# Kernel tuning notes

Hardware: AMD Instinct MI355X
Metric: run time of the kernel (lower is better)

## Reference

```python
import math
import jax, jax.numpy as jnp
import numpy as np

B, N, M = 8, 2048, 1024
INPUT_SIZE = 512
HEAD_DIM = 64
NUM_HEADS = 6
ATTN_SIZE = HEAD_DIM * NUM_HEADS
MAX_CLASSES = 512


def setup_inputs() -> dict:
    key = jax.random.key(0)
    k1, k2, k3, k4, k5, k6, k7 = jax.random.split(key, 7)
    bound = 1.0 / math.sqrt(INPUT_SIZE)
    return {
        "train_embeddings": jax.random.normal(k1, (B, N, INPUT_SIZE), jnp.float32),
        "test_embeddings": jax.random.normal(k2, (B, M, INPUT_SIZE), jnp.float32),
        "targets": jax.random.randint(k3, (B, N), 0, MAX_CLASSES),
        # torch nn.Linear weights, stored as [in, out] for direct matmul
        "Wq": jax.random.uniform(k4, (INPUT_SIZE, ATTN_SIZE), jnp.float32, -bound, bound),
        "bq": jax.random.uniform(k5, (ATTN_SIZE,), jnp.float32, -bound, bound),
        "Wk": jax.random.uniform(k6, (INPUT_SIZE, ATTN_SIZE), jnp.float32, -bound, bound),
        "bk": jax.random.uniform(k7, (ATTN_SIZE,), jnp.float32, -bound, bound),
    }


def reference(train_embeddings, test_embeddings, targets, Wq, bq, Wk, bk):
    b, m, _ = test_embeddings.shape
    # projections -> [B, S, H, D]
    q_bmhd = (test_embeddings @ Wq + bq).reshape(b, m, NUM_HEADS, HEAD_DIM)
    k_bnhd = (train_embeddings @ Wk + bk).reshape(b, -1, NUM_HEADS, HEAD_DIM)
    scale = 1.0 / math.sqrt(HEAD_DIM)  # SDPA default scale
    # attention scores [B, H, M, N]
    scores = jnp.einsum("bmhd,bnhd->bhmn", q_bmhd, k_bnhd) * scale
    attn = jax.nn.softmax(scores, axis=-1)
    # one-hot train targets [B, N, C]; chunk-folding in the torch code is a
    # memory trick — mathematically it is just attn @ one_hot per head
    onehot_bnc = jax.nn.one_hot(targets, MAX_CLASSES, dtype=q_bmhd.dtype)
    out_bhmc = jnp.einsum("bhmn,bnc->bhmc", attn, onehot_bnc)
    out_bmc = out_bhmc.mean(axis=1)          # mean over heads
    out_mbc = out_bmc.transpose(1, 0, 2)      # [M, B, C]
    return jnp.log(jnp.clip(out_mbc, 1e-05) + 3e-05)
```

## Files before the change

### kernel.cpp

```cpp
#include <hip/hip_runtime.h>
#include <hip/hip_bf16.h>

#define BQ 8
#define NN 2048
#define MM 1024
#define EE 512
#define NH 6
#define AA 384
#define CC 512

#define KROW_B (AA * 2)
#define TILE_B (16 * KROW_B)
#define STILE_B (32 * KROW_B)
#define WROW_B (EE * 2)
#define WTILE_B (16 * WROW_B)

#define QSCALE 0.1803368801111204f

typedef __bf16 bf16x8 __attribute__((ext_vector_type(8)));
typedef float  f32x4  __attribute__((ext_vector_type(4)));
using bf16 = __hip_bfloat16;

static __device__ __forceinline__ f32x4 mfma16(bf16x8 a, bf16x8 b, f32x4 c) {
  return __builtin_amdgcn_mfma_f32_16x16x32_bf16(a, b, c, 0, 0, 0);
}

typedef __attribute__((address_space(1))) const void gconst_void;
typedef __attribute__((address_space(3))) void lds_void_t;
static __device__ __forceinline__ void ld_lds16(const void* g, void* l) {
  __builtin_amdgcn_global_load_lds((gconst_void*)g, (lds_void_t*)l, 16, 0, 0);
}

static __device__ __forceinline__ unsigned short f2bfu(float x) {
  union { __hip_bfloat16 h; unsigned short u; } v;
  v.h = __float2bfloat16(x);
  return v.u;
}
static __device__ __forceinline__ float bf2f(unsigned short u) {
  union { unsigned int i; float f; } x;
  x.i = ((unsigned int)u) << 16;
  return x.f;
}

__global__ __launch_bounds__(512) void prep_kernel(
    const float* __restrict__ Wq, const float* __restrict__ Wk,
    bf16* __restrict__ WqT, bf16* __restrict__ WkT,
    const int* __restrict__ targets, int* __restrict__ cnts, int* __restrict__ idxP)
{
  __shared__ float t[64][65];
  __shared__ int cnt[CC], pos[CC];
  int bid = blockIdx.x, tid = threadIdx.x;
  if (bid < 96) {
    if (tid >= 256) { __syncthreads(); return; }
    int id = bid;
    const float* W = (id < 48) ? Wq : Wk;
    bf16* WT = (id < 48) ? WqT : WkT;
    if (id >= 48) id -= 48;
    int kb = (id / 6) * 64, nb = (id % 6) * 64;
    int lr = tid >> 4, lc = (tid & 15) * 4;
    #pragma unroll
    for (int p = 0; p < 4; p++) {
      int k = lr + p * 16;
      float4 v = *reinterpret_cast<const float4*>(W + (size_t)(kb + k) * AA + nb + lc);
      t[k][lc] = v.x; t[k][lc + 1] = v.y; t[k][lc + 2] = v.z; t[k][lc + 3] = v.w;
    }
    __syncthreads();
    #pragma unroll
    for (int p = 0; p < 4; p++) {
      int n = lr + p * 16;
      bf16* dst = WT + (size_t)(nb + n) * EE + kb + lc;
      dst[0] = __float2bfloat16(t[lc][n]);
      dst[1] = __float2bfloat16(t[lc + 1][n]);
      dst[2] = __float2bfloat16(t[lc + 2][n]);
      dst[3] = __float2bfloat16(t[lc + 3][n]);
    }
    return;
  }
  int b = bid - 96;
  cnt[tid] = 0;
  pos[tid] = 0;
  int4 sent = make_int4(NN, NN, NN, NN);
  int4* prow = reinterpret_cast<int4*>(idxP + ((size_t)b * CC + tid) * 32);
  #pragma unroll
  for (int i = 0; i < 8; i++) prow[i] = sent;
  __syncthreads();
  int tv[4];
  #pragma unroll
  for (int i = 0; i < 4; i++) {
    tv[i] = targets[b * NN + tid * 4 + i];
    atomicAdd(&cnt[tv[i]], 1);
  }
  __syncthreads();
  cnts[b * CC + tid] = cnt[tid];
  __syncthreads();
  #pragma unroll
  for (int i = 0; i < 4; i++) {
    int p = atomicAdd(&pos[tv[i]], 1);
    if (p < 32) idxP[((size_t)b * CC + tv[i]) * 32 + p] = tid * 4 + i;
  }
}

__global__ __launch_bounds__(256, 3) void proj_kernel(
    const float* __restrict__ test, const float* __restrict__ train,
    const bf16* __restrict__ WqT, const bf16* __restrict__ WkT,
    const float* __restrict__ bq, const float* __restrict__ bk,
    bf16* __restrict__ Qb, bf16* __restrict__ Kb)
{
  __shared__ char wbuf[3][WTILE_B];
  int tid = threadIdx.x, wid = tid >> 6, lane = tid & 63;
  int bid = blockIdx.x;
  int sub = bid & 1, unit = bid >> 1;
  const float* A; const bf16* WT; const float* bias; bf16* C; float scale; int m0;
  if (unit < 128) { A = test;  WT = WqT; bias = bq; C = Qb; scale = QSCALE; m0 = unit * 64; }
  else            { A = train; WT = WkT; bias = bk; C = Kb; scale = 1.0f;   m0 = (unit - 128) * 64; }
  m0 += wid * 16;
  int row = lane & 15, hi = lane >> 4;

  bf16x8 af[16];
  const float* arow = A + (size_t)(m0 + row) * EE + hi * 8;
  #pragma unroll
  for (int ks = 0; ks < 16; ks++) {
    float4 u = *reinterpret_cast<const float4*>(arow + ks * 32);
    float4 v = *reinterpret_cast<const float4*>(arow + ks * 32 + 4);
    bf16x8 f;
    f[0] = (__bf16)u.x; f[1] = (__bf16)u.y; f[2] = (__bf16)u.z; f[3] = (__bf16)u.w;
    f[4] = (__bf16)v.x; f[5] = (__bf16)v.y; f[6] = (__bf16)v.z; f[7] = (__bf16)v.w;
    af[ks] = f;
  }

  int ldso[4], srco[4];
  #pragma unroll
  for (int i = 0; i < 4; i++) {
    int off = tid * 16 + i * 4096;
    int rw = off >> 10, c = off & 1023;
    ldso[i] = off;
    srco[i] = rw * WROW_B + (c ^ ((rw & 7) << 4));
  }
  const char* wgbase = (const char*)WT + (size_t)sub * 12 * WTILE_B;
  int sw = (row & 7) << 4;

  auto stage = [&](int t, int buf) {
    const char* src = wgbase + (size_t)t * WTILE_B;
    #pragma unroll
    for (int i = 0; i < 4; i++) ld_lds16(src + srco[i], wbuf[buf] + ldso[i]);
  };
  auto compute = [&](int buf, int t) {
    const char* wb = wbuf[buf] + row * WROW_B;
    f32x4 acc0 = {0.f, 0.f, 0.f, 0.f}, acc1 = {0.f, 0.f, 0.f, 0.f};
    #pragma unroll
    for (int ks = 0; ks < 16; ks += 2) {
      bf16x8 w0 = *reinterpret_cast<const bf16x8*>(wb + ((hi * 16 + ks * 64) ^ sw));
      bf16x8 w1 = *reinterpret_cast<const bf16x8*>(wb + ((hi * 16 + (ks + 1) * 64) ^ sw));
      acc0 = mfma16(af[ks], w0, acc0);
      acc1 = mfma16(af[ks + 1], w1, acc1);
    }
    f32x4 acc = acc0 + acc1;
    int ocol = (sub * 12 + t) * 16 + row;
    float bv = bias[ocol];
    #pragma unroll
    for (int j = 0; j < 4; j++)
      C[(size_t)(m0 + hi * 4 + j) * AA + ocol] = __float2bfloat16((acc[j] + bv) * scale);
  };

  stage(0, 0);
  stage(1, 1);
  asm volatile("s_waitcnt vmcnt(4)" ::: "memory");
  __builtin_amdgcn_s_barrier();
  __builtin_amdgcn_sched_barrier(0);
  stage(2, 2);
  compute(0, 0);

  int cur = 1, stg = 0;
  #pragma unroll 1
  for (int t = 1; t < 11; t++) {
    asm volatile("s_waitcnt vmcnt(8)" ::: "memory");
    __builtin_amdgcn_s_barrier();
    __builtin_amdgcn_sched_barrier(0);
    if (t < 10) stage(t + 2, stg);
    compute(cur, t);
    cur = cur + 1 < 3 ? cur + 1 : 0;
    stg = stg + 1 < 3 ? stg + 1 : 0;
  }
  asm volatile("s_waitcnt vmcnt(4)" ::: "memory");
  __builtin_amdgcn_s_barrier();
  __builtin_amdgcn_sched_barrier(0);
  compute(cur, 11);
}

__global__ __launch_bounds__(256, 2) void zpass_kernel(
    const bf16* __restrict__ Qb, const bf16* __restrict__ Kb, float* __restrict__ Zp)
{
  __shared__ char kbuf[2][STILE_B];
  int id = blockIdx.x;
  int b = id & 7, r = id >> 3, mt = r & 7, nc = r >> 3;
  int tid = threadIdx.x, wid = tid >> 6, lane = tid & 63;
  int m0 = mt * 128 + wid * 32, n0 = nc * 256;
  int row = lane & 15, hi = lane >> 4;

  bf16x8 qf[2][12];
  #pragma unroll
  for (int s = 0; s < 2; s++) {
    const bf16* qrow = Qb + ((size_t)(b * MM + m0 + s * 16 + row)) * AA + hi * 8;
    #pragma unroll
    for (int ks = 0; ks < 12; ks++) qf[s][ks] = *reinterpret_cast<const bf16x8*>(qrow + ks * 32);
  }

  int ldso[6], srco[6];
  #pragma unroll
  for (int i = 0; i < 6; i++) {
    int off = tid * 16 + i * 4096;
    int rw = off / KROW_B, c = off - rw * KROW_B;
    ldso[i] = off;
    srco[i] = rw * KROW_B + (c ^ ((rw & 7) << 4));
  }
  const char* kgbase = (const char*)(Kb + ((size_t)(b * NN + n0)) * AA);

  int sw = (row & 7) << 4;
  int rbase = row * KROW_B;
  int x0 = rbase + ((hi * 16) ^ sw);
  int x1 = rbase + (((hi * 16) + 64) ^ sw);

  float zacc[2][NH][4];
  #pragma unroll
  for (int s = 0; s < 2; s++)
    #pragma unroll
    for (int h = 0; h < NH; h++)
      #pragma unroll
      for (int j = 0; j < 4; j++) zacc[s][h][j] = 0.f;

  auto stage = [&](int t, int buf) {
    const char* src = kgbase + (size_t)t * STILE_B;
    #pragma unroll
    for (int i = 0; i < 6; i++) ld_lds16(src + srco[i], kbuf[buf] + ldso[i]);
  };
  auto compute = [&](int buf) {
    __builtin_amdgcn_s_setprio(1);
    #pragma unroll
    for (int sub = 0; sub < 2; sub++) {
      const char* kb = kbuf[buf] + sub * TILE_B;
      #pragma unroll
      for (int h = 0; h < NH; h++) {
        bf16x8 k0 = *reinterpret_cast<const bf16x8*>(kb + h * 128 + x0);
        bf16x8 k1 = *reinterpret_cast<const bf16x8*>(kb + h * 128 + x1);
        f32x4 a0 = {0.f, 0.f, 0.f, 0.f}, a1 = {0.f, 0.f, 0.f, 0.f};
        a0 = mfma16(qf[0][2 * h], k0, a0);
        a1 = mfma16(qf[1][2 * h], k0, a1);
        a0 = mfma16(qf[0][2 * h + 1], k1, a0);
        a1 = mfma16(qf[1][2 * h + 1], k1, a1);
        #pragma unroll
        for (int j = 0; j < 4; j++) {
          zacc[0][h][j] += __builtin_amdgcn_exp2f(a0[j]);
          zacc[1][h][j] += __builtin_amdgcn_exp2f(a1[j]);
        }
      }
    }
    __builtin_amdgcn_s_setprio(0);
  };

  stage(0, 0);
  asm volatile("s_waitcnt vmcnt(0)" ::: "memory");
  __builtin_amdgcn_s_barrier();
  __builtin_amdgcn_sched_barrier(0);
  stage(1, 1);
  compute(0);

  #pragma unroll 1
  for (int i = 1; i < 8; i++) {
    asm volatile("s_waitcnt vmcnt(0)" ::: "memory");
    __builtin_amdgcn_s_barrier();
    __builtin_amdgcn_sched_barrier(0);
    if (i < 7) stage(i + 1, (i + 1) & 1);
    compute(i & 1);
  }

  #pragma unroll
  for (int s = 0; s < 2; s++)
    #pragma unroll
    for (int h = 0; h < NH; h++)
      #pragma unroll
      for (int j = 0; j < 4; j++) {
        float v = zacc[s][h][j];
        v += __shfl_xor(v, 1); v += __shfl_xor(v, 2);
        v += __shfl_xor(v, 4); v += __shfl_xor(v, 8);
        zacc[s][h][j] = v;
      }
  if (row == 0) {
    #pragma unroll
    for (int s = 0; s < 2; s++)
      #pragma unroll
      for (int h = 0; h < NH; h++)
        #pragma unroll
        for (int j = 0; j < 4; j++)
          Zp[(((size_t)nc * 8 + b) * NH + h) * MM + m0 + s * 16 + hi * 4 + j] = zacc[s][h][j];
  }
}

__global__ __launch_bounds__(256, 2) void wpass_kernel(
    const bf16* __restrict__ Qb, const bf16* __restrict__ Kb,
    const float* __restrict__ Zp, bf16* __restrict__ W2)
{
  __shared__ char kbuf[2][STILE_B];
  int id = blockIdx.x;
  int b = id & 7, r = id >> 3, mt = r & 7, nc = r >> 3;
  int tid = threadIdx.x, wid = tid >> 6, lane = tid & 63;
  int m0 = mt * 128 + wid * 32, n0 = nc * 256;
  int row = lane & 15, hi = lane >> 4;

  bf16x8 qf[2][12];
  #pragma unroll
  for (int s = 0; s < 2; s++) {
    const bf16* qrow = Qb + ((size_t)(b * MM + m0 + s * 16 + row)) * AA + hi * 8;
    #pragma unroll
    for (int ks = 0; ks < 12; ks++) qf[s][ks] = *reinterpret_cast<const bf16x8*>(qrow + ks * 32);
  }

  f32x4 lrz4[2][NH];
  #pragma unroll
  for (int s = 0; s < 2; s++)
    #pragma unroll
    for (int h = 0; h < NH; h++) {
      f32x4 z = {0.f, 0.f, 0.f, 0.f};
      #pragma unroll
      for (int p = 0; p < 8; p++)
        z += *reinterpret_cast<const f32x4*>(Zp + (((size_t)p * 8 + b) * NH + h) * MM + m0 + s * 16 + hi * 4);
      f32x4 l;
      #pragma unroll
      for (int j = 0; j < 4; j++) l[j] = -__log2f(6.0f * z[j]);
      lrz4[s][h] = l;
    }

  int ldso[6], srco[6];
  #pragma unroll
  for (int i = 0; i < 6; i++) {
    int off = tid * 16 + i * 4096;
    int rw = off / KROW_B, c = off - rw * KROW_B;
    ldso[i] = off;
    srco[i] = rw * KROW_B + (c ^ ((rw & 7) << 4));
  }
  const char* kgbase = (const char*)(Kb + ((size_t)(b * NN + n0)) * AA);

  int sw = (row & 7) << 4;
  int rbase = row * KROW_B;
  int x0 = rbase + ((hi * 16) ^ sw);
  int x1 = rbase + (((hi * 16) + 64) ^ sw);

  int m4a = (m0 >> 2) + hi;
  int m4b = ((m0 + 16) >> 2) + hi;

  auto stage = [&](int t, int buf) {
    const char* src = kgbase + (size_t)t * STILE_B;
    #pragma unroll
    for (int i = 0; i < 6; i++) ld_lds16(src + srco[i], kbuf[buf] + ldso[i]);
  };
  auto compute = [&](int buf, int st) {
    #pragma unroll
    for (int sub = 0; sub < 2; sub++) {
      const char* kb = kbuf[buf] + sub * TILE_B;
      __builtin_amdgcn_s_setprio(1);
      float w0a = 0.f, w1a = 0.f, w2a = 0.f, w3a = 0.f;
      float w0b = 0.f, w1b = 0.f, w2b = 0.f, w3b = 0.f;
      #pragma unroll
      for (int h = 0; h < NH; h++) {
        bf16x8 k0 = *reinterpret_cast<const bf16x8*>(kb + h * 128 + x0);
        bf16x8 k1 = *reinterpret_cast<const bf16x8*>(kb + h * 128 + x1);
        f32x4 a0 = mfma16(qf[0][2 * h], k0, lrz4[0][h]);
        f32x4 a1 = mfma16(qf[1][2 * h], k0, lrz4[1][h]);
        a0 = mfma16(qf[0][2 * h + 1], k1, a0);
        a1 = mfma16(qf[1][2 * h + 1], k1, a1);
        w0a += __builtin_amdgcn_exp2f(a0[0]);
        w1a += __builtin_amdgcn_exp2f(a0[1]);
        w2a += __builtin_amdgcn_exp2f(a0[2]);
        w3a += __builtin_amdgcn_exp2f(a0[3]);
        w0b += __builtin_amdgcn_exp2f(a1[0]);
        w1b += __builtin_amdgcn_exp2f(a1[1]);
        w2b += __builtin_amdgcn_exp2f(a1[2]);
        w3b += __builtin_amdgcn_exp2f(a1[3]);
      }
      __builtin_amdgcn_s_setprio(0);
      int n = n0 + (st * 2 + sub) * 16 + row;
      ushort4 qa, qb2;
      qa.x = f2bfu(w0a); qa.y = f2bfu(w1a); qa.z = f2bfu(w2a); qa.w = f2bfu(w3a);
      qb2.x = f2bfu(w0b); qb2.y = f2bfu(w1b); qb2.z = f2bfu(w2b); qb2.w = f2bfu(w3b);
      *reinterpret_cast<ushort4*>((unsigned short*)W2 + (((size_t)(b * 256 + m4a)) * NN + n) * 4) = qa;
      *reinterpret_cast<ushort4*>((unsigned short*)W2 + (((size_t)(b * 256 + m4b)) * NN + n) * 4) = qb2;
    }
  };

  stage(0, 0);
  asm volatile("s_waitcnt vmcnt(0)" ::: "memory");
  __builtin_amdgcn_s_barrier();
  __builtin_amdgcn_sched_barrier(0);
  stage(1, 1);
  compute(0, 0);

  #pragma unroll 1
  for (int i = 1; i < 8; i++) {
    asm volatile("s_waitcnt vmcnt(4)" ::: "memory");
    __builtin_amdgcn_s_barrier();
    __builtin_amdgcn_sched_barrier(0);
    if (i < 7) stage(i + 1, (i + 1) & 1);
    compute(i & 1, i);
  }
}

__global__ __launch_bounds__(512) void gather_kernel(
    const bf16* __restrict__ W2, const int* __restrict__ cnts,
    const int* __restrict__ idxP, float* __restrict__ out)
{
  __shared__ char wl[2 * (NN + 1) * 8];
  int id = blockIdx.x;
  int b = id & 7, mt = id >> 3;
  int g0 = mt * 2;
  int tid = threadIdx.x;

  #pragma unroll
  for (int g = 0; g < 2; g++) {
    const uint4* src = (const uint4*)((const unsigned short*)W2 + ((size_t)(b * 256 + g0 + g)) * NN * 4);
    uint4* dst = (uint4*)(wl + g * (NN + 1) * 8);
    #pragma unroll
    for (int i = tid; i < NN * 8 / 16; i += 512) dst[i] = src[i];
  }
  if (tid < 2) *reinterpret_cast<unsigned long long*>(wl + tid * (NN + 1) * 8 + NN * 8) = 0ull;
  __syncthreads();

  int c = tid;
  int cnt = cnts[b * CC + c];
  const int* ip = idxP + ((size_t)b * CC + c) * 32;
  #pragma unroll 1
  for (int g = 0; g < 2; g++) {
    const char* base = wl + g * (NN + 1) * 8;
    float s0 = 0.f, s1 = 0.f, s2 = 0.f, s3 = 0.f;
    #pragma unroll 1
    for (int i = 0; i < cnt; i += 8) {
      int4 ia = *reinterpret_cast<const int4*>(ip + i);
      int4 ib = *reinterpret_cast<const int4*>(ip + i + 4);
      ushort4 v0 = *reinterpret_cast<const ushort4*>(base + ia.x * 8);
      ushort4 v1 = *reinterpret_cast<const ushort4*>(base + ia.y * 8);
      ushort4 v2 = *reinterpret_cast<const ushort4*>(base + ia.z * 8);
      ushort4 v3 = *reinterpret_cast<const ushort4*>(base + ia.w * 8);
      ushort4 v4 = *reinterpret_cast<const ushort4*>(base + ib.x * 8);
      ushort4 v5 = *reinterpret_cast<const ushort4*>(base + ib.y * 8);
      ushort4 v6 = *reinterpret_cast<const ushort4*>(base + ib.z * 8);
      ushort4 v7 = *reinterpret_cast<const ushort4*>(base + ib.w * 8);
      s0 += bf2f(v0.x) + bf2f(v1.x) + bf2f(v2.x) + bf2f(v3.x) + bf2f(v4.x) + bf2f(v5.x) + bf2f(v6.x) + bf2f(v7.x);
      s1 += bf2f(v0.y) + bf2f(v1.y) + bf2f(v2.y) + bf2f(v3.y) + bf2f(v4.y) + bf2f(v5.y) + bf2f(v6.y) + bf2f(v7.y);
      s2 += bf2f(v0.z) + bf2f(v1.z) + bf2f(v2.z) + bf2f(v3.z) + bf2f(v4.z) + bf2f(v5.z) + bf2f(v6.z) + bf2f(v7.z);
      s3 += bf2f(v0.w) + bf2f(v1.w) + bf2f(v2.w) + bf2f(v3.w) + bf2f(v4.w) + bf2f(v5.w) + bf2f(v6.w) + bf2f(v7.w);
    }
    int m = mt * 8 + g * 4;
    out[((size_t)(m + 0) * BQ + b) * CC + c] = __logf(fmaxf(s0, 1e-5f) + 3e-5f);
    out[((size_t)(m + 1) * BQ + b) * CC + c] = __logf(fmaxf(s1, 1e-5f) + 3e-5f);
    out[((size_t)(m + 2) * BQ + b) * CC + c] = __logf(fmaxf(s2, 1e-5f) + 3e-5f);
    out[((size_t)(m + 3) * BQ + b) * CC + c] = __logf(fmaxf(s3, 1e-5f) + 3e-5f);
  }
}

extern "C" void kernel_launch(void* const* d_in, const int* in_sizes, int n_in,
                              void* d_out, int out_size, void* d_ws, size_t ws_size,
                              hipStream_t stream) {
  const float* train = (const float*)d_in[0];
  const float* test  = (const float*)d_in[1];
  const int*   tgt   = (const int*)d_in[2];
  const float* Wq    = (const float*)d_in[3];
  const float* bq    = (const float*)d_in[4];
  const float* Wk    = (const float*)d_in[5];
  const float* bk    = (const float*)d_in[6];
  float* out = (float*)d_out;

  char* ws = (char*)d_ws;
  bf16*  WqT  = (bf16*)(ws);
  bf16*  WkT  = (bf16*)(ws + 393216);
  bf16*  Qb   = (bf16*)(ws + 786432);
  bf16*  Kb   = (bf16*)(ws + 7077888);
  float* Zp   = (float*)(ws + 19660800);
  bf16*  Wbuf = (bf16*)(ws + 21233664);
  int*   cnts = (int*)(ws + 54788096);
  int*   idxP = (int*)(ws + 54804480);

  prep_kernel<<<104, 512, 0, stream>>>(Wq, Wk, WqT, WkT, tgt, cnts, idxP);
  proj_kernel<<<768, 256, 0, stream>>>(test, train, WqT, WkT, bq, bk, Qb, Kb);
  zpass_kernel<<<512, 256, 0, stream>>>(Qb, Kb, Zp);
  wpass_kernel<<<512, 256, 0, stream>>>(Qb, Kb, Zp, Wbuf);
  gather_kernel<<<1024, 512, 0, stream>>>(Wbuf, cnts, idxP, out);
}
```

Measured before the change: 107.3 us.

## Shrink zpass/wpass blocks to 2 waves with triple-buffered 16-row K tiles

The zpass and wpass kernels now launch twice as many blocks of 128 threads, each covering 64 query rows instead of 128. Each iteration stages a 16-row K tile instead of 32 rows, over a 3-deep LDS ring with partial vmcnt waits, so loads run two tiles ahead of compute. The aim is more resident blocks, finer-grained barriers and better latency hiding. The cost is that each K tile is reloaded by twice as many blocks, raising global/L2 traffic for K.

```diff
diff --git a/kernel.cpp b/kernel.cpp
--- a/kernel.cpp
+++ b/kernel.cpp
@@ -11,7 +11,6 @@
 
 #define KROW_B (AA * 2)
 #define TILE_B (16 * KROW_B)
-#define STILE_B (32 * KROW_B)
 #define WROW_B (EE * 2)
 #define WTILE_B (16 * WROW_B)
 
@@ -187,14 +186,14 @@
   compute(cur, 11);
 }
 
-__global__ __launch_bounds__(256, 2) void zpass_kernel(
+__global__ __launch_bounds__(128) void zpass_kernel(
     const bf16* __restrict__ Qb, const bf16* __restrict__ Kb, float* __restrict__ Zp)
 {
-  __shared__ char kbuf[2][STILE_B];
+  __shared__ char kbuf[3][TILE_B];
   int id = blockIdx.x;
-  int b = id & 7, r = id >> 3, mt = r & 7, nc = r >> 3;
+  int b = id & 7, r = id >> 3, mt = r & 15, nc = r >> 4;
   int tid = threadIdx.x, wid = tid >> 6, lane = tid & 63;
-  int m0 = mt * 128 + wid * 32, n0 = nc * 256;
+  int m0 = mt * 64 + wid * 32, n0 = nc * 256;
   int row = lane & 15, hi = lane >> 4;
 
   bf16x8 qf[2][12];
@@ -208,7 +207,7 @@
   int ldso[6], srco[6];
   #pragma unroll
   for (int i = 0; i < 6; i++) {
-    int off = tid * 16 + i * 4096;
+    int off = tid * 16 + i * 2048;
     int rw = off / KROW_B, c = off - rw * KROW_B;
     ldso[i] = off;
     srco[i] = rw * KROW_B + (c ^ ((rw & 7) << 4));
@@ -229,49 +228,54 @@
       for (int j = 0; j < 4; j++) zacc[s][h][j] = 0.f;
 
   auto stage = [&](int t, int buf) {
-    const char* src = kgbase + (size_t)t * STILE_B;
+    const char* src = kgbase + (size_t)t * TILE_B;
     #pragma unroll
     for (int i = 0; i < 6; i++) ld_lds16(src + srco[i], kbuf[buf] + ldso[i]);
   };
   auto compute = [&](int buf) {
+    const char* kb = kbuf[buf];
     __builtin_amdgcn_s_setprio(1);
     #pragma unroll
-    for (int sub = 0; sub < 2; sub++) {
-      const char* kb = kbuf[buf] + sub * TILE_B;
-      #pragma unroll
-      for (int h = 0; h < NH; h++) {
-        bf16x8 k0 = *reinterpret_cast<const bf16x8*>(kb + h * 128 + x0);
-        bf16x8 k1 = *reinterpret_cast<const bf16x8*>(kb + h * 128 + x1);
-        f32x4 a0 = {0.f, 0.f, 0.f, 0.f}, a1 = {0.f, 0.f, 0.f, 0.f};
-        a0 = mfma16(qf[0][2 * h], k0, a0);
-        a1 = mfma16(qf[1][2 * h], k0, a1);
-        a0 = mfma16(qf[0][2 * h + 1], k1, a0);
-        a1 = mfma16(qf[1][2 * h + 1], k1, a1);
-        #pragma unroll
-        for (int j = 0; j < 4; j++) {
-          zacc[0][h][j] += __builtin_amdgcn_exp2f(a0[j]);
-          zacc[1][h][j] += __builtin_amdgcn_exp2f(a1[j]);
-        }
+    for (int h = 0; h < NH; h++) {
+      bf16x8 k0 = *reinterpret_cast<const bf16x8*>(kb + h * 128 + x0);
+      bf16x8 k1 = *reinterpret_cast<const bf16x8*>(kb + h * 128 + x1);
+      f32x4 a0 = {0.f, 0.f, 0.f, 0.f}, a1 = {0.f, 0.f, 0.f, 0.f};
+      a0 = mfma16(qf[0][2 * h], k0, a0);
+      a1 = mfma16(qf[1][2 * h], k0, a1);
+      a0 = mfma16(qf[0][2 * h + 1], k1, a0);
+      a1 = mfma16(qf[1][2 * h + 1], k1, a1);
+      #pragma unroll
+      for (int j = 0; j < 4; j++) {
+        zacc[0][h][j] += __builtin_amdgcn_exp2f(a0[j]);
+        zacc[1][h][j] += __builtin_amdgcn_exp2f(a1[j]);
       }
     }
     __builtin_amdgcn_s_setprio(0);
   };
 
   stage(0, 0);
-  asm volatile("s_waitcnt vmcnt(0)" ::: "memory");
-  __builtin_amdgcn_s_barrier();
-  __builtin_amdgcn_sched_barrier(0);
   stage(1, 1);
+  asm volatile("s_waitcnt vmcnt(6)" ::: "memory");
+  __builtin_amdgcn_s_barrier();
+  __builtin_amdgcn_sched_barrier(0);
+  stage(2, 2);
   compute(0);
 
+  int cur = 1, stg = 0;
   #pragma unroll 1
-  for (int i = 1; i < 8; i++) {
-    asm volatile("s_waitcnt vmcnt(0)" ::: "memory");
+  for (int i = 1; i < 15; i++) {
+    asm volatile("s_waitcnt vmcnt(6)" ::: "memory");
     __builtin_amdgcn_s_barrier();
     __builtin_amdgcn_sched_barrier(0);
-    if (i < 7) stage(i + 1, (i + 1) & 1);
-    compute(i & 1);
-  }
+    if (i < 14) stage(i + 2, stg);
+    compute(cur);
+    cur = cur + 1 < 3 ? cur + 1 : 0;
+    stg = stg + 1 < 3 ? stg + 1 : 0;
+  }
+  asm volatile("s_waitcnt vmcnt(0)" ::: "memory");
+  __builtin_amdgcn_s_barrier();
+  __builtin_amdgcn_sched_barrier(0);
+  compute(cur);
 
   #pragma unroll
   for (int s = 0; s < 2; s++)
@@ -295,15 +299,15 @@
   }
 }
 
-__global__ __launch_bounds__(256, 2) void wpass_kernel(
+__global__ __launch_bounds__(128) void wpass_kernel(
     const bf16* __restrict__ Qb, const bf16* __restrict__ Kb,
     const float* __restrict__ Zp, bf16* __restrict__ W2)
 {
-  __shared__ char kbuf[2][STILE_B];
+  __shared__ char kbuf[3][TILE_B];
   int id = blockIdx.x;
-  int b = id & 7, r = id >> 3, mt = r & 7, nc = r >> 3;
+  int b = id & 7, r = id >> 3, mt = r & 15, nc = r >> 4;
   int tid = threadIdx.x, wid = tid >> 6, lane = tid & 63;
-  int m0 = mt * 128 + wid * 32, n0 = nc * 256;
+  int m0 = mt * 64 + wid * 32, n0 = nc * 256;
   int row = lane & 15, hi = lane >> 4;
 
   bf16x8 qf[2][12];
@@ -332,7 +336,7 @@
   int ldso[6], srco[6];
   #pragma unroll
   for (int i = 0; i < 6; i++) {
-    int off = tid * 16 + i * 4096;
+    int off = tid * 16 + i * 2048;
     int rw = off / KROW_B, c = off - rw * KROW_B;
     ldso[i] = off;
     srco[i] = rw * KROW_B + (c ^ ((rw & 7) << 4));
@@ -348,59 +352,64 @@
   int m4b = ((m0 + 16) >> 2) + hi;
 
   auto stage = [&](int t, int buf) {
-    const char* src = kgbase + (size_t)t * STILE_B;
+    const char* src = kgbase + (size_t)t * TILE_B;
     #pragma unroll
     for (int i = 0; i < 6; i++) ld_lds16(src + srco[i], kbuf[buf] + ldso[i]);
   };
-  auto compute = [&](int buf, int st) {
-    #pragma unroll
-    for (int sub = 0; sub < 2; sub++) {
-      const char* kb = kbuf[buf] + sub * TILE_B;
-      __builtin_amdgcn_s_setprio(1);
-      float w0a = 0.f, w1a = 0.f, w2a = 0.f, w3a = 0.f;
-      float w0b = 0.f, w1b = 0.f, w2b = 0.f, w3b = 0.f;
-      #pragma unroll
-      for (int h = 0; h < NH; h++) {
-        bf16x8 k0 = *reinterpret_cast<const bf16x8*>(kb + h * 128 + x0);
-        bf16x8 k1 = *reinterpret_cast<const bf16x8*>(kb + h * 128 + x1);
-        f32x4 a0 = mfma16(qf[0][2 * h], k0, lrz4[0][h]);
-        f32x4 a1 = mfma16(qf[1][2 * h], k0, lrz4[1][h]);
-        a0 = mfma16(qf[0][2 * h + 1], k1, a0);
-        a1 = mfma16(qf[1][2 * h + 1], k1, a1);
-        w0a += __builtin_amdgcn_exp2f(a0[0]);
-        w1a += __builtin_amdgcn_exp2f(a0[1]);
-        w2a += __builtin_amdgcn_exp2f(a0[2]);
-        w3a += __builtin_amdgcn_exp2f(a0[3]);
-        w0b += __builtin_amdgcn_exp2f(a1[0]);
-        w1b += __builtin_amdgcn_exp2f(a1[1]);
-        w2b += __builtin_amdgcn_exp2f(a1[2]);
-        w3b += __builtin_amdgcn_exp2f(a1[3]);
-      }
-      __builtin_amdgcn_s_setprio(0);
-      int n = n0 + (st * 2 + sub) * 16 + row;
-      ushort4 qa, qb2;
-      qa.x = f2bfu(w0a); qa.y = f2bfu(w1a); qa.z = f2bfu(w2a); qa.w = f2bfu(w3a);
-      qb2.x = f2bfu(w0b); qb2.y = f2bfu(w1b); qb2.z = f2bfu(w2b); qb2.w = f2bfu(w3b);
-      *reinterpret_cast<ushort4*>((unsigned short*)W2 + (((size_t)(b * 256 + m4a)) * NN + n) * 4) = qa;
-      *reinterpret_cast<ushort4*>((unsigned short*)W2 + (((size_t)(b * 256 + m4b)) * NN + n) * 4) = qb2;
-    }
+  auto compute = [&](int buf, int t) {
+    const char* kb = kbuf[buf];
+    __builtin_amdgcn_s_setprio(1);
+    float w0a = 0.f, w1a = 0.f, w2a = 0.f, w3a = 0.f;
+    float w0b = 0.f, w1b = 0.f, w2b = 0.f, w3b = 0.f;
+    #pragma unroll
+    for (int h = 0; h < NH; h++) {
+      bf16x8 k0 = *reinterpret_cast<const bf16x8*>(kb + h * 128 + x0);
+      bf16x8 k1 = *reinterpret_cast<const bf16x8*>(kb + h * 128 + x1);
+      f32x4 a0 = mfma16(qf[0][2 * h], k0, lrz4[0][h]);
+      f32x4 a1 = mfma16(qf[1][2 * h], k0, lrz4[1][h]);
+      a0 = mfma16(qf[0][2 * h + 1], k1, a0);
+      a1 = mfma16(qf[1][2 * h + 1], k1, a1);
+      w0a += __builtin_amdgcn_exp2f(a0[0]);
+      w1a += __builtin_amdgcn_exp2f(a0[1]);
+      w2a += __builtin_amdgcn_exp2f(a0[2]);
+      w3a += __builtin_amdgcn_exp2f(a0[3]);
+      w0b += __builtin_amdgcn_exp2f(a1[0]);
+      w1b += __builtin_amdgcn_exp2f(a1[1]);
+      w2b += __builtin_amdgcn_exp2f(a1[2]);
+      w3b += __builtin_amdgcn_exp2f(a1[3]);
+    }
+    __builtin_amdgcn_s_setprio(0);
+    int n = n0 + t * 16 + row;
+    ushort4 qa, qb2;
+    qa.x = f2bfu(w0a); qa.y = f2bfu(w1a); qa.z = f2bfu(w2a); qa.w = f2bfu(w3a);
+    qb2.x = f2bfu(w0b); qb2.y = f2bfu(w1b); qb2.z = f2bfu(w2b); qb2.w = f2bfu(w3b);
+    *reinterpret_cast<ushort4*>((unsigned short*)W2 + (((size_t)(b * 256 + m4a)) * NN + n) * 4) = qa;
+    *reinterpret_cast<ushort4*>((unsigned short*)W2 + (((size_t)(b * 256 + m4b)) * NN + n) * 4) = qb2;
   };
 
   stage(0, 0);
-  asm volatile("s_waitcnt vmcnt(0)" ::: "memory");
-  __builtin_amdgcn_s_barrier();
-  __builtin_amdgcn_sched_barrier(0);
   stage(1, 1);
+  asm volatile("s_waitcnt vmcnt(6)" ::: "memory");
+  __builtin_amdgcn_s_barrier();
+  __builtin_amdgcn_sched_barrier(0);
+  stage(2, 2);
   compute(0, 0);
 
+  int cur = 1, stg = 0;
   #pragma unroll 1
-  for (int i = 1; i < 8; i++) {
-    asm volatile("s_waitcnt vmcnt(4)" ::: "memory");
+  for (int i = 1; i < 15; i++) {
+    asm volatile("s_waitcnt vmcnt(8)" ::: "memory");
     __builtin_amdgcn_s_barrier();
     __builtin_amdgcn_sched_barrier(0);
-    if (i < 7) stage(i + 1, (i + 1) & 1);
-    compute(i & 1, i);
-  }
+    if (i < 14) stage(i + 2, stg);
+    compute(cur, i);
+    cur = cur + 1 < 3 ? cur + 1 : 0;
+    stg = stg + 1 < 3 ? stg + 1 : 0;
+  }
+  asm volatile("s_waitcnt vmcnt(4)" ::: "memory");
+  __builtin_amdgcn_s_barrier();
+  __builtin_amdgcn_sched_barrier(0);
+  compute(cur, 15);
 }
 
 __global__ __launch_bounds__(512) void gather_kernel(
@@ -479,7 +488,7 @@
 
   prep_kernel<<<104, 512, 0, stream>>>(Wq, Wk, WqT, WkT, tgt, cnts, idxP);
   proj_kernel<<<768, 256, 0, stream>>>(test, train, WqT, WkT, bq, bk, Qb, Kb);
-  zpass_kernel<<<512, 256, 0, stream>>>(Qb, Kb, Zp);
-  wpass_kernel<<<512, 256, 0, stream>>>(Qb, Kb, Zp, Wbuf);
+  zpass_kernel<<<1024, 128, 0, stream>>>(Qb, Kb, Zp);
+  wpass_kernel<<<1024, 128, 0, stream>>>(Qb, Kb, Zp, Wbuf);
   gather_kernel<<<1024, 512, 0, stream>>>(Wbuf, cnts, idxP, out);
 }
```

After: 120.0 us. 1.12x slower.

## Merge score passes into one fp8 unnormalized-weight pass with normalization in gather

Applied to the files above, without the earlier changes.

The separate Z-sum pass and normalized-weight pass are replaced by one pass. It writes unnormalized exp2 scores per head as fp8 for every (m,n) pair, and the gather kernel now derives the per-head softmax denominators by summing over all classes before normalizing. This removes one full QK^T recomputation, but the intermediate grows to 8 bytes per (m,n) covering all M rows (about 134MB), where before four query rows were packed per element. It also relies on unscaled fp8 holding the exp values without overflow or precision loss, and the gather launch count quadruples.

```diff
diff --git a/kernel.cpp b/kernel.cpp
--- a/kernel.cpp
+++ b/kernel.cpp
@@ -31,15 +31,41 @@
   __builtin_amdgcn_global_load_lds((gconst_void*)g, (lds_void_t*)l, 16, 0, 0);
 }
 
-static __device__ __forceinline__ unsigned short f2bfu(float x) {
-  union { __hip_bfloat16 h; unsigned short u; } v;
-  v.h = __float2bfloat16(x);
-  return v.u;
-}
-static __device__ __forceinline__ float bf2f(unsigned short u) {
-  union { unsigned int i; float f; } x;
-  x.i = ((unsigned int)u) << 16;
-  return x.f;
+static __device__ __forceinline__ unsigned enc_fp8(float f) {
+  unsigned b = __float_as_uint(f) + 0x00080000u;
+  int e = (int)((b >> 23) & 0xFF) - 120;
+  if (e <= 0) return 0u;
+  if (e >= 16) return 0x7Eu;
+  return ((unsigned)e << 3) | ((b >> 20) & 7u);
+}
+static __device__ __forceinline__ float dec_fp8(unsigned u) {
+  unsigned e = (u >> 3) & 0xFu;
+  if (e == 0) return 0.f;
+  return __uint_as_float(((e + 120u) << 23) | ((u & 7u) << 20));
+}
+static __device__ __forceinline__ unsigned pk4(float a, float b, float c, float d) {
+#if __has_builtin(__builtin_amdgcn_cvt_pk_fp8_f32)
+  int v = __builtin_amdgcn_cvt_pk_fp8_f32(a, b, 0, false);
+  v = __builtin_amdgcn_cvt_pk_fp8_f32(c, d, v, true);
+  return (unsigned)v;
+#else
+  return enc_fp8(a) | (enc_fp8(b) << 8) | (enc_fp8(c) << 16) | (enc_fp8(d) << 24);
+#endif
+}
+static __device__ __forceinline__ unsigned pk2(float a, float b) {
+#if __has_builtin(__builtin_amdgcn_cvt_pk_fp8_f32)
+  return (unsigned)__builtin_amdgcn_cvt_pk_fp8_f32(a, b, 0, false);
+#else
+  return enc_fp8(a) | (enc_fp8(b) << 8);
+#endif
+}
+template <int SEL>
+static __device__ __forceinline__ float up8(unsigned d) {
+#if __has_builtin(__builtin_amdgcn_cvt_f32_fp8)
+  return __builtin_amdgcn_cvt_f32_fp8((int)d, SEL);
+#else
+  return dec_fp8((d >> (SEL * 8)) & 0xFFu);
+#endif
 }
 
 __global__ __launch_bounds__(512) void prep_kernel(
@@ -187,8 +213,8 @@
   compute(cur, 11);
 }
 
-__global__ __launch_bounds__(256, 2) void zpass_kernel(
-    const bf16* __restrict__ Qb, const bf16* __restrict__ Kb, float* __restrict__ Zp)
+__global__ __launch_bounds__(256, 2) void spass_kernel(
+    const bf16* __restrict__ Qb, const bf16* __restrict__ Kb, char* __restrict__ Wh)
 {
   __shared__ char kbuf[2][STILE_B];
   int id = blockIdx.x;
@@ -220,24 +246,17 @@
   int x0 = rbase + ((hi * 16) ^ sw);
   int x1 = rbase + (((hi * 16) + 64) ^ sw);
 
-  float zacc[2][NH][4];
-  #pragma unroll
-  for (int s = 0; s < 2; s++)
-    #pragma unroll
-    for (int h = 0; h < NH; h++)
-      #pragma unroll
-      for (int j = 0; j < 4; j++) zacc[s][h][j] = 0.f;
-
   auto stage = [&](int t, int buf) {
     const char* src = kgbase + (size_t)t * STILE_B;
     #pragma unroll
     for (int i = 0; i < 6; i++) ld_lds16(src + srco[i], kbuf[buf] + ldso[i]);
   };
-  auto compute = [&](int buf) {
-    __builtin_amdgcn_s_setprio(1);
+  auto compute = [&](int buf, int st) {
     #pragma unroll
     for (int sub = 0; sub < 2; sub++) {
       const char* kb = kbuf[buf] + sub * TILE_B;
+      float w[2][NH][4];
+      __builtin_amdgcn_s_setprio(1);
       #pragma unroll
       for (int h = 0; h < NH; h++) {
         bf16x8 k0 = *reinterpret_cast<const bf16x8*>(kb + h * 128 + x0);
@@ -249,140 +268,21 @@
         a1 = mfma16(qf[1][2 * h + 1], k1, a1);
         #pragma unroll
         for (int j = 0; j < 4; j++) {
-          zacc[0][h][j] += __builtin_amdgcn_exp2f(a0[j]);
-          zacc[1][h][j] += __builtin_amdgcn_exp2f(a1[j]);
+          w[0][h][j] = __builtin_amdgcn_exp2f(a0[j]);
+          w[1][h][j] = __builtin_amdgcn_exp2f(a1[j]);
         }
-      }
-    }
-    __builtin_amdgcn_s_setprio(0);
-  };
-
-  stage(0, 0);
-  asm volatile("s_waitcnt vmcnt(0)" ::: "memory");
-  __builtin_amdgcn_s_barrier();
-  __builtin_amdgcn_sched_barrier(0);
-  stage(1, 1);
-  compute(0);
-
-  #pragma unroll 1
-  for (int i = 1; i < 8; i++) {
-    asm volatile("s_waitcnt vmcnt(0)" ::: "memory");
-    __builtin_amdgcn_s_barrier();
-    __builtin_amdgcn_sched_barrier(0);
-    if (i < 7) stage(i + 1, (i + 1) & 1);
-    compute(i & 1);
-  }
-
-  #pragma unroll
-  for (int s = 0; s < 2; s++)
-    #pragma unroll
-    for (int h = 0; h < NH; h++)
-      #pragma unroll
-      for (int j = 0; j < 4; j++) {
-        float v = zacc[s][h][j];
-        v += __shfl_xor(v, 1); v += __shfl_xor(v, 2);
-        v += __shfl_xor(v, 4); v += __shfl_xor(v, 8);
-        zacc[s][h][j] = v;
-      }
-  if (row == 0) {
-    #pragma unroll
-    for (int s = 0; s < 2; s++)
-      #pragma unroll
-      for (int h = 0; h < NH; h++)
-        #pragma unroll
-        for (int j = 0; j < 4; j++)
-          Zp[(((size_t)nc * 8 + b) * NH + h) * MM + m0 + s * 16 + hi * 4 + j] = zacc[s][h][j];
-  }
-}
-
-__global__ __launch_bounds__(256, 2) void wpass_kernel(
-    const bf16* __restrict__ Qb, const bf16* __restrict__ Kb,
-    const float* __restrict__ Zp, bf16* __restrict__ W2)
-{
-  __shared__ char kbuf[2][STILE_B];
-  int id = blockIdx.x;
-  int b = id & 7, r = id >> 3, mt = r & 7, nc = r >> 3;
-  int tid = threadIdx.x, wid = tid >> 6, lane = tid & 63;
-  int m0 = mt * 128 + wid * 32, n0 = nc * 256;
-  int row = lane & 15, hi = lane >> 4;
-
-  bf16x8 qf[2][12];
-  #pragma unroll
-  for (int s = 0; s < 2; s++) {
-    const bf16* qrow = Qb + ((size_t)(b * MM + m0 + s * 16 + row)) * AA + hi * 8;
-    #pragma unroll
-    for (int ks = 0; ks < 12; ks++) qf[s][ks] = *reinterpret_cast<const bf16x8*>(qrow + ks * 32);
-  }
-
-  f32x4 lrz4[2][NH];
-  #pragma unroll
-  for (int s = 0; s < 2; s++)
-    #pragma unroll
-    for (int h = 0; h < NH; h++) {
-      f32x4 z = {0.f, 0.f, 0.f, 0.f};
-      #pragma unroll
-      for (int p = 0; p < 8; p++)
-        z += *reinterpret_cast<const f32x4*>(Zp + (((size_t)p * 8 + b) * NH + h) * MM + m0 + s * 16 + hi * 4);
-      f32x4 l;
-      #pragma unroll
-      for (int j = 0; j < 4; j++) l[j] = -__log2f(6.0f * z[j]);
-      lrz4[s][h] = l;
-    }
-
-  int ldso[6], srco[6];
-  #pragma unroll
-  for (int i = 0; i < 6; i++) {
-    int off = tid * 16 + i * 4096;
-    int rw = off / KROW_B, c = off - rw * KROW_B;
-    ldso[i] = off;
-    srco[i] = rw * KROW_B + (c ^ ((rw & 7) << 4));
-  }
-  const char* kgbase = (const char*)(Kb + ((size_t)(b * NN + n0)) * AA);
-
-  int sw = (row & 7) << 4;
-  int rbase = row * KROW_B;
-  int x0 = rbase + ((hi * 16) ^ sw);
-  int x1 = rbase + (((hi * 16) + 64) ^ sw);
-
-  int m4a = (m0 >> 2) + hi;
-  int m4b = ((m0 + 16) >> 2) + hi;
-
-  auto stage = [&](int t, int buf) {
-    const char* src = kgbase + (size_t)t * STILE_B;
-    #pragma unroll
-    for (int i = 0; i < 6; i++) ld_lds16(src + srco[i], kbuf[buf] + ldso[i]);
-  };
-  auto compute = [&](int buf, int st) {
-    #pragma unroll
-    for (int sub = 0; sub < 2; sub++) {
-      const char* kb = kbuf[buf] + sub * TILE_B;
-      __builtin_amdgcn_s_setprio(1);
-      float w0a = 0.f, w1a = 0.f, w2a = 0.f, w3a = 0.f;
-      float w0b = 0.f, w1b = 0.f, w2b = 0.f, w3b = 0.f;
-      #pragma unroll
-      for (int h = 0; h < NH; h++) {
-        bf16x8 k0 = *reinterpret_cast<const bf16x8*>(kb + h * 128 + x0);
-        bf16x8 k1 = *reinterpret_cast<const bf16x8*>(kb + h * 128 + x1);
-        f32x4 a0 = mfma16(qf[0][2 * h], k0, lrz4[0][h]);
-        f32x4 a1 = mfma16(qf[1][2 * h], k0, lrz4[1][h]);
-        a0 = mfma16(qf[0][2 * h + 1], k1, a0);
-        a1 = mfma16(qf[1][2 * h + 1], k1, a1);
-        w0a += __builtin_amdgcn_exp2f(a0[0]);
-        w1a += __builtin_amdgcn_exp2f(a0[1]);
-        w2a += __builtin_amdgcn_exp2f(a0[2]);
-        w3a += __builtin_amdgcn_exp2f(a0[3]);
-        w0b += __builtin_amdgcn_exp2f(a1[0]);
-        w1b += __builtin_amdgcn_exp2f(a1[1]);
-        w2b += __builtin_amdgcn_exp2f(a1[2]);
-        w3b += __builtin_amdgcn_exp2f(a1[3]);
       }
       __builtin_amdgcn_s_setprio(0);
       int n = n0 + (st * 2 + sub) * 16 + row;
-      ushort4 qa, qb2;
-      qa.x = f2bfu(w0a); qa.y = f2bfu(w1a); qa.z = f2bfu(w2a); qa.w = f2bfu(w3a);
-      qb2.x = f2bfu(w0b); qb2.y = f2bfu(w1b); qb2.z = f2bfu(w2b); qb2.w = f2bfu(w3b);
-      *reinterpret_cast<ushort4*>((unsigned short*)W2 + (((size_t)(b * 256 + m4a)) * NN + n) * 4) = qa;
-      *reinterpret_cast<ushort4*>((unsigned short*)W2 + (((size_t)(b * 256 + m4b)) * NN + n) * 4) = qb2;
+      #pragma unroll
+      for (int s = 0; s < 2; s++)
+        #pragma unroll
+        for (int j = 0; j < 4; j++) {
+          unsigned d0 = pk4(w[s][0][j], w[s][1][j], w[s][2][j], w[s][3][j]);
+          unsigned d1 = pk2(w[s][4][j], w[s][5][j]);
+          int m = m0 + s * 16 + hi * 4 + j;
+          *reinterpret_cast<uint2*>(Wh + (((size_t)(b * MM + m)) * NN + n) * 8) = make_uint2(d0, d1);
+        }
     }
   };
 
@@ -395,7 +295,7 @@
 
   #pragma unroll 1
   for (int i = 1; i < 8; i++) {
-    asm volatile("s_waitcnt vmcnt(4)" ::: "memory");
+    asm volatile("s_waitcnt vmcnt(16)" ::: "memory");
     __builtin_amdgcn_s_barrier();
     __builtin_amdgcn_sched_barrier(0);
     if (i < 7) stage(i + 1, (i + 1) & 1);
@@ -404,54 +304,78 @@
 }
 
 __global__ __launch_bounds__(512) void gather_kernel(
-    const bf16* __restrict__ W2, const int* __restrict__ cnts,
+    const char* __restrict__ Wh, const int* __restrict__ cnts,
     const int* __restrict__ idxP, float* __restrict__ out)
 {
-  __shared__ char wl[2 * (NN + 1) * 8];
+  __shared__ uint2 wl[2][2050];
+  __shared__ float wred[8][12];
+  __shared__ float rzs[12];
   int id = blockIdx.x;
   int b = id & 7, mt = id >> 3;
-  int g0 = mt * 2;
-  int tid = threadIdx.x;
-
-  #pragma unroll
-  for (int g = 0; g < 2; g++) {
-    const uint4* src = (const uint4*)((const unsigned short*)W2 + ((size_t)(b * 256 + g0 + g)) * NN * 4);
-    uint4* dst = (uint4*)(wl + g * (NN + 1) * 8);
-    #pragma unroll
-    for (int i = tid; i < NN * 8 / 16; i += 512) dst[i] = src[i];
-  }
-  if (tid < 2) *reinterpret_cast<unsigned long long*>(wl + tid * (NN + 1) * 8 + NN * 8) = 0ull;
+  int m0 = mt * 2;
+  int tid = threadIdx.x, wid = tid >> 6, lane = tid & 63;
+
+  #pragma unroll
+  for (int m = 0; m < 2; m++) {
+    const uint4* src = (const uint4*)(Wh + ((size_t)(b * MM + m0 + m) * NN) * 8);
+    uint4* dst = (uint4*)&wl[m][0];
+    #pragma unroll 2
+    for (int i = tid; i < NN / 2; i += 512) dst[i] = src[i];
+  }
+  if (tid < 2) wl[tid][2048] = make_uint2(0u, 0u);
   __syncthreads();
 
   int c = tid;
-  int cnt = cnts[b * CC + c];
+  int kc = cnts[b * CC + c];
   const int* ip = idxP + ((size_t)b * CC + c) * 32;
+  float B[2][NH];
+  #pragma unroll
+  for (int m = 0; m < 2; m++)
+    #pragma unroll
+    for (int h = 0; h < NH; h++) B[m][h] = 0.f;
+
+  int kcp = (kc + 3) & ~3;
   #pragma unroll 1
-  for (int g = 0; g < 2; g++) {
-    const char* base = wl + g * (NN + 1) * 8;
-    float s0 = 0.f, s1 = 0.f, s2 = 0.f, s3 = 0.f;
-    #pragma unroll 1
-    for (int i = 0; i < cnt; i += 8) {
-      int4 ia = *reinterpret_cast<const int4*>(ip + i);
-      int4 ib = *reinterpret_cast<const int4*>(ip + i + 4);
-      ushort4 v0 = *reinterpret_cast<const ushort4*>(base + ia.x * 8);
-      ushort4 v1 = *reinterpret_cast<const ushort4*>(base + ia.y * 8);
-      ushort4 v2 = *reinterpret_cast<const ushort4*>(base + ia.z * 8);
-      ushort4 v3 = *reinterpret_cast<const ushort4*>(base + ia.w * 8);
-      ushort4 v4 = *reinterpret_cast<const ushort4*>(base + ib.x * 8);
-      ushort4 v5 = *reinterpret_cast<const ushort4*>(base + ib.y * 8);
-      ushort4 v6 = *reinterpret_cast<const ushort4*>(base + ib.z * 8);
-      ushort4 v7 = *reinterpret_cast<const ushort4*>(base + ib.w * 8);
-      s0 += bf2f(v0.x) + bf2f(v1.x) + bf2f(v2.x) + bf2f(v3.x) + bf2f(v4.x) + bf2f(v5.x) + bf2f(v6.x) + bf2f(v7.x);
-      s1 += bf2f(v0.y) + bf2f(v1.y) + bf2f(v2.y) + bf2f(v3.y) + bf2f(v4.y) + bf2f(v5.y) + bf2f(v6.y) + bf2f(v7.y);
-      s2 += bf2f(v0.z) + bf2f(v1.z) + bf2f(v2.z) + bf2f(v3.z) + bf2f(v4.z) + bf2f(v5.z) + bf2f(v6.z) + bf2f(v7.z);
-      s3 += bf2f(v0.w) + bf2f(v1.w) + bf2f(v2.w) + bf2f(v3.w) + bf2f(v4.w) + bf2f(v5.w) + bf2f(v6.w) + bf2f(v7.w);
-    }
-    int m = mt * 8 + g * 4;
-    out[((size_t)(m + 0) * BQ + b) * CC + c] = __logf(fmaxf(s0, 1e-5f) + 3e-5f);
-    out[((size_t)(m + 1) * BQ + b) * CC + c] = __logf(fmaxf(s1, 1e-5f) + 3e-5f);
-    out[((size_t)(m + 2) * BQ + b) * CC + c] = __logf(fmaxf(s2, 1e-5f) + 3e-5f);
-    out[((size_t)(m + 3) * BQ + b) * CC + c] = __logf(fmaxf(s3, 1e-5f) + 3e-5f);
+  for (int i = 0; i < kcp; i += 4) {
+    int4 ia = *reinterpret_cast<const int4*>(ip + i);
+    int idxs4[4] = {ia.x, ia.y, ia.z, ia.w};
+    #pragma unroll
+    for (int e = 0; e < 4; e++) {
+      int idx = idxs4[e];
+      #pragma unroll
+      for (int m = 0; m < 2; m++) {
+        uint2 v = wl[m][idx];
+        B[m][0] += up8<0>(v.x); B[m][1] += up8<1>(v.x);
+        B[m][2] += up8<2>(v.x); B[m][3] += up8<3>(v.x);
+        B[m][4] += up8<0>(v.y); B[m][5] += up8<1>(v.y);
+      }
+    }
+  }
+
+  #pragma unroll
+  for (int m = 0; m < 2; m++)
+    #pragma unroll
+    for (int h = 0; h < NH; h++) {
+      float t = B[m][h];
+      t += __shfl_xor(t, 1);  t += __shfl_xor(t, 2);  t += __shfl_xor(t, 4);
+      t += __shfl_xor(t, 8);  t += __shfl_xor(t, 16); t += __shfl_xor(t, 32);
+      if (lane == 0) wred[wid][m * NH + h] = t;
+    }
+  __syncthreads();
+  if (tid < 12) {
+    float z = 0.f;
+    #pragma unroll
+    for (int w = 0; w < 8; w++) z += wred[w][tid];
+    rzs[tid] = 1.0f / (6.0f * z);
+  }
+  __syncthreads();
+
+  #pragma unroll
+  for (int m = 0; m < 2; m++) {
+    float v = 0.f;
+    #pragma unroll
+    for (int h = 0; h < NH; h++) v += B[m][h] * rzs[m * NH + h];
+    out[((size_t)(m0 + m) * BQ + b) * CC + c] = __logf(fmaxf(v, 1e-5f) + 3e-5f);
   }
 }
 
@@ -472,14 +396,12 @@
   bf16*  WkT  = (bf16*)(ws + 393216);
   bf16*  Qb   = (bf16*)(ws + 786432);
   bf16*  Kb   = (bf16*)(ws + 7077888);
-  float* Zp   = (float*)(ws + 19660800);
-  bf16*  Wbuf = (bf16*)(ws + 21233664);
-  int*   cnts = (int*)(ws + 54788096);
-  int*   idxP = (int*)(ws + 54804480);
+  char*  Wh   = (char*)(ws + 19660800);
+  int*   cnts = (int*)(ws + 153878528);
+  int*   idxP = (int*)(ws + 153894912);
 
   prep_kernel<<<104, 512, 0, stream>>>(Wq, Wk, WqT, WkT, tgt, cnts, idxP);
   proj_kernel<<<768, 256, 0, stream>>>(test, train, WqT, WkT, bq, bk, Qb, Kb);
-  zpass_kernel<<<512, 256, 0, stream>>>(Qb, Kb, Zp);
-  wpass_kernel<<<512, 256, 0, stream>>>(Qb, Kb, Zp, Wbuf);
-  gather_kernel<<<1024, 512, 0, stream>>>(Wbuf, cnts, idxP, out);
-}
+  spass_kernel<<<512, 256, 0, stream>>>(Qb, Kb, Wh);
+  gather_kernel<<<4096, 512, 0, stream>>>(Wh, cnts, idxP, out);
+}
```

Measured after the change: 109.2 us. About the same (+1.8%).
